# Optimization experiments

Measured on AMD Instinct MI355X. Metric: run time of the kernel, lower is better.

The kernel has to match this reference:

```python
import jax, jax.numpy as jnp
import numpy as np

B, N, T, C, H = 4, 1024, 32, 256, 8
LN_EPS = 1e-5


def setup_inputs() -> dict:
    key = jax.random.key(0)
    ks = jax.random.split(key, 10)
    BN = B * N
    x = jax.random.normal(ks[0], (BN, T, C), dtype=jnp.float32)
    # frame timestamps, sorted increasing, moderate scale so decay bias is meaningful
    timestamps = jnp.sort(jax.random.uniform(ks[1], (B, T), dtype=jnp.float32) * 64.0, axis=1)
    s = 0.02
    params = {
        'ln_gamma': jnp.ones((C,), jnp.float32),
        'ln_beta': jnp.zeros((C,), jnp.float32),
        'Wq': jax.random.normal(ks[2], (C, C), jnp.float32) * s,
        'bq': jnp.zeros((C,), jnp.float32),
        'Wk': jax.random.normal(ks[3], (C, C), jnp.float32) * s,
        'Wv': jax.random.normal(ks[4], (C, C), jnp.float32) * s,
        'Wg': jax.random.normal(ks[5], (C, C), jnp.float32) * s,
        # out_proj is zero-init in the module; use small random here so output is non-trivial
        'Wo': jax.random.normal(ks[6], (C, C), jnp.float32) * s,
        'log_lambda': jnp.linspace(np.log(0.004), np.log(0.7), H).astype(jnp.float32),
    }
    return {'x': x, 'timestamps': timestamps, 'n_spatial': N, **params}


def reference(x, timestamps, n_spatial, ln_gamma, ln_beta, Wq, bq, Wk, Wv, Wg, Wo, log_lambda):
    BN, T_, C_ = x.shape
    Bb = BN // n_spatial
    Hh = log_lambda.shape[0]
    d = C_ // Hh

    # LayerNorm
    mu = jnp.mean(x, axis=-1, keepdims=True)
    var = jnp.mean(jnp.square(x - mu), axis=-1, keepdims=True)
    h = (x - mu) * jax.lax.rsqrt(var + LN_EPS) * ln_gamma + ln_beta

    q = (h @ Wq.T + bq).reshape(BN, T_, Hh, d)
    k = (h @ Wk.T).reshape(BN, T_, Hh, d)
    v = (h @ Wv.T).reshape(BN, T_, Hh, d)
    g = jax.nn.sigmoid(h @ Wg.T)

    # temporal decay bias: (B, H, T, T), broadcast over spatial positions
    dt = jnp.abs(timestamps[:, :, None] - timestamps[:, None, :])  # (B,T,T)
    bias = -jnp.exp(log_lambda)[None, :, None, None] * dt[:, None, :, :]  # (B,H,T,T)

    scores = jnp.einsum('bthd,bshd->bhts', q.astype(jnp.float32), k.astype(jnp.float32))
    scores = scores / jnp.sqrt(jnp.float32(d))
    # broadcast bias instead of repeat_interleave: (B, N, H, T, T)
    scores = scores.reshape(Bb, n_spatial, Hh, T_, T_) + bias[:, None]
    attn = jax.nn.softmax(scores, axis=-1).reshape(BN, Hh, T_, T_)

    o = jnp.einsum('bhts,bshd->bthd', attn, v.astype(jnp.float32)).astype(v.dtype)
    o = o.reshape(BN, T_, C_)
    return x + (g * o) @ Wo.T
```

## Files before the change

kernel.cpp:

```cpp
#include <hip/hip_runtime.h>
#include <hip/hip_bf16.h>


typedef __attribute__((ext_vector_type(8))) short  s16x8;
typedef __attribute__((ext_vector_type(4))) float  f32x4;
typedef __attribute__((ext_vector_type(4))) unsigned short us16x4;

#define MFMA16(a, b, c) __builtin_amdgcn_mfma_f32_16x16x32_bf16((a), (b), (c), 0, 0, 0)

static __device__ __forceinline__ unsigned short f2bfu(float f) {
  __hip_bfloat16 h = __float2bfloat16(f);
  return __builtin_bit_cast(unsigned short, h);
}
static __device__ __forceinline__ unsigned pack2(float lo, float hi) {
  return (unsigned)f2bfu(lo) | ((unsigned)f2bfu(hi) << 16);
}
static __device__ __forceinline__ float bf_lo(unsigned u) {
  union { unsigned u; float f; } v; v.u = u << 16; return v.f;
}
static __device__ __forceinline__ float bf_hi(unsigned u) {
  union { unsigned u; float f; } v; v.u = u & 0xFFFF0000u; return v.f;
}

#define RS      528
#define ZSTR    72
#define LDS_A   0
#define LDS_TS  16896
#define LDS_Z   17024
#define ZONE    4608
#define LDS_TOTAL (LDS_Z + 4 * ZONE)

#define WS_WQ   0
#define WS_WK   131072
#define WS_WV   262144
#define WS_WG   393216
#define WS_WO   524288
#define WS_LAM  655360

__global__ void prep_kernel(const float* __restrict__ Wq, const float* __restrict__ Wk,
                            const float* __restrict__ Wv, const float* __restrict__ Wg,
                            const float* __restrict__ Wo, const float* __restrict__ ll,
                            char* __restrict__ ws) {
  int tid = blockIdx.x * 256 + threadIdx.x;
  if (tid < 5 * 8192) {
    int m      = tid >> 13;
    int within = tid & 8191;
    int lane   = within & 63;
    int j = 16 * (within >> 9) + (lane & 15);
    int c = 32 * ((within >> 6) & 7) + 8 * (lane >> 4);
    const float* W = (m == 0) ? Wq : (m == 1) ? Wk : (m == 2) ? Wv : (m == 3) ? Wg : Wo;
    const float* src = W + j * 256 + c;
    s16x8 o;
#pragma unroll
    for (int i = 0; i < 8; ++i) o[i] = (short)f2bfu(src[i]);
    *(s16x8*)(ws + (size_t)tid * 16) = o;
  } else if (tid < 5 * 8192 + 8) {
    ((float*)(ws + WS_LAM))[tid - 40960] = __expf(ll[tid - 40960]);
  }
}

template <int NT>
static __device__ __forceinline__ void gemmNT(const char* lds, const char* wmat,
                                              int ntg0, int lane, f32x4 acc[2][NT]) {
  const int l15 = lane & 15, l4 = lane >> 4;
  const s16x8* Bf = (const s16x8*)wmat + ntg0 * 8 * 64 + lane;
  s16x8 b[NT][8];
#pragma unroll
  for (int nt = 0; nt < NT; ++nt)
#pragma unroll
    for (int ks = 0; ks < 8; ++ks) b[nt][ks] = Bf[(nt * 8 + ks) * 64];
#pragma unroll
  for (int mt = 0; mt < 2; ++mt)
#pragma unroll
    for (int nt = 0; nt < NT; ++nt) acc[mt][nt] = (f32x4){0.f, 0.f, 0.f, 0.f};
#pragma unroll
  for (int ks = 0; ks < 8; ++ks) {
    s16x8 a[2];
#pragma unroll
    for (int mt = 0; mt < 2; ++mt)
      a[mt] = *(const s16x8*)(lds + LDS_A + (16 * mt + l15) * RS + 64 * ks + 16 * l4);
#pragma unroll
    for (int nt = 0; nt < NT; ++nt)
#pragma unroll
      for (int mt = 0; mt < 2; ++mt) acc[mt][nt] = MFMA16(a[mt], b[nt][ks], acc[mt][nt]);
  }
}

__global__ __launch_bounds__(256, 3) void fused_kernel(
    const float* __restrict__ x, const float* __restrict__ tsg,
    const float* __restrict__ gamma, const float* __restrict__ beta,
    const float* __restrict__ bq, const char* __restrict__ ws,
    float* __restrict__ out) {
  extern __shared__ __align__(16) char lds[];
  const int tid = threadIdx.x;
  const int lane = tid & 63;
  const int w = tid >> 6;
  const int l15 = lane & 15, l4 = lane >> 4;
  const int blk = blockIdx.x;
  char* zA = lds + LDS_Z + w * ZONE;
  char* zB = zA + 2304;

  {
    const int r = tid >> 3, sub = tid & 7;
    const float* xr = x + ((size_t)blk * 32 + r) * 256 + sub * 32;
    float4 xv[8];
    float s = 0.f, s2 = 0.f;
#pragma unroll
    for (int u = 0; u < 8; ++u) {
      xv[u] = *(const float4*)(xr + 4 * u);
      s  += xv[u].x + xv[u].y + xv[u].z + xv[u].w;
      s2 += xv[u].x * xv[u].x + xv[u].y * xv[u].y + xv[u].z * xv[u].z + xv[u].w * xv[u].w;
    }
#pragma unroll
    for (int m = 1; m <= 4; m <<= 1) { s += __shfl_xor(s, m); s2 += __shfl_xor(s2, m); }
    float mu = s * (1.f / 256.f);
    float rstd = rsqrtf(s2 * (1.f / 256.f) - mu * mu + 1e-5f);
#pragma unroll
    for (int u = 0; u < 8; ++u) {
      int c = sub * 32 + 4 * u;
      float4 gv = *(const float4*)(gamma + c);
      float4 bv = *(const float4*)(beta + c);
      us16x4 hb;
      hb[0] = f2bfu((xv[u].x - mu) * rstd * gv.x + bv.x);
      hb[1] = f2bfu((xv[u].y - mu) * rstd * gv.y + bv.y);
      hb[2] = f2bfu((xv[u].z - mu) * rstd * gv.z + bv.z);
      hb[3] = f2bfu((xv[u].w - mu) * rstd * gv.w + bv.w);
      *(us16x4*)(lds + LDS_A + r * RS + 2 * c) = hb;
    }
    if (tid < 32) ((float*)(lds + LDS_TS))[tid] = tsg[(blk >> 10) * 32 + tid];
  }
  __syncthreads();

  const float* tsl = (const float*)(lds + LDS_TS);
  const float* lam = (const float*)(ws + WS_LAM);
  const float tc0 = tsl[l15], tc1 = tsl[l15 + 16];
  float trow[8];
#pragma unroll
  for (int mh = 0; mh < 2; ++mh)
#pragma unroll
    for (int r = 0; r < 4; ++r) trow[mh * 4 + r] = tsl[16 * mh + 4 * l4 + r];
  const f32x4 zf = {0.f, 0.f, 0.f, 0.f};
  unsigned gopk[2][2][2][2];

#pragma unroll
  for (int hp = 0; hp < 2; ++hp) {
    const int h = 2 * w + hp;
    f32x4 acc[2][2];
    unsigned gpk[2][2][2];

    gemmNT<2>(lds, ws + WS_WG, 2 * h, lane, acc);
#pragma unroll
    for (int mt = 0; mt < 2; ++mt)
#pragma unroll
      for (int nt = 0; nt < 2; ++nt)
#pragma unroll
        for (int rp = 0; rp < 2; ++rp)
          gpk[mt][nt][rp] = pack2(1.f / (1.f + __expf(-acc[mt][nt][2 * rp])),
                                  1.f / (1.f + __expf(-acc[mt][nt][2 * rp + 1])));

    gemmNT<2>(lds, ws + WS_WV, 2 * h, lane, acc);
#pragma unroll
    for (int mt = 0; mt < 2; ++mt)
#pragma unroll
      for (int nt = 0; nt < 2; ++nt)
#pragma unroll
        for (int rp = 0; rp < 2; ++rp)
          *(unsigned*)(zB + (16 * nt + l15) * ZSTR + 2 * (16 * mt + 4 * l4 + 2 * rp)) =
              pack2(acc[mt][nt][2 * rp], acc[mt][nt][2 * rp + 1]);

    gemmNT<2>(lds, ws + WS_WK, 2 * h, lane, acc);
#pragma unroll
    for (int mt = 0; mt < 2; ++mt)
#pragma unroll
      for (int nt = 0; nt < 2; ++nt)
#pragma unroll
        for (int r = 0; r < 4; ++r)
          *(short*)(zA + (16 * mt + 4 * l4 + r) * ZSTR + 2 * (16 * nt + l15)) =
              (short)f2bfu(acc[mt][nt][r]);
    s16x8 bk0 = *(const s16x8*)(zA + l15 * ZSTR + 16 * l4);
    s16x8 bk1 = *(const s16x8*)(zA + (16 + l15) * ZSTR + 16 * l4);

    gemmNT<2>(lds, ws + WS_WQ, 2 * h, lane, acc);
    {
      float bq0 = bq[32 * h + l15], bq1 = bq[32 * h + 16 + l15];
#pragma unroll
      for (int mt = 0; mt < 2; ++mt)
#pragma unroll
        for (int nt = 0; nt < 2; ++nt)
#pragma unroll
          for (int r = 0; r < 4; ++r)
            *(short*)(zA + (16 * mt + 4 * l4 + r) * ZSTR + 2 * (16 * nt + l15)) =
                (short)f2bfu((acc[mt][nt][r] + (nt ? bq1 : bq0)) * 0.17677669529663687f);
    }
    s16x8 aq0 = *(const s16x8*)(zA + l15 * ZSTR + 16 * l4);
    s16x8 aq1 = *(const s16x8*)(zA + (16 + l15) * ZSTR + 16 * l4);

    f32x4 sc[2][2];
    sc[0][0] = MFMA16(aq0, bk0, zf);
    sc[0][1] = MFMA16(aq0, bk1, zf);
    sc[1][0] = MFMA16(aq1, bk0, zf);
    sc[1][1] = MFMA16(aq1, bk1, zf);

    const float lamh = lam[h];
#pragma unroll
    for (int mh = 0; mh < 2; ++mh)
#pragma unroll
      for (int r = 0; r < 4; ++r) {
        float tr = trow[mh * 4 + r];
        float a0 = sc[mh][0][r] - lamh * fabsf(tr - tc0);
        float a1 = sc[mh][1][r] - lamh * fabsf(tr - tc1);
        float m = fmaxf(a0, a1);
        m = fmaxf(m, __shfl_xor(m, 1)); m = fmaxf(m, __shfl_xor(m, 2));
        m = fmaxf(m, __shfl_xor(m, 4)); m = fmaxf(m, __shfl_xor(m, 8));
        float e0 = __expf(a0 - m), e1 = __expf(a1 - m);
        float su = e0 + e1;
        su += __shfl_xor(su, 1); su += __shfl_xor(su, 2);
        su += __shfl_xor(su, 4); su += __shfl_xor(su, 8);
        float inv = 1.0f / su;
        int t = 16 * mh + 4 * l4 + r;
        *(short*)(zA + t * ZSTR + 2 * l15)        = (short)f2bfu(e0 * inv);
        *(short*)(zA + t * ZSTR + 2 * (l15 + 16)) = (short)f2bfu(e1 * inv);
      }

    s16x8 ap0 = *(const s16x8*)(zA + l15 * ZSTR + 16 * l4);
    s16x8 ap1 = *(const s16x8*)(zA + (16 + l15) * ZSTR + 16 * l4);
    s16x8 bv0 = *(const s16x8*)(zB + l15 * ZSTR + 16 * l4);
    s16x8 bv1 = *(const s16x8*)(zB + (16 + l15) * ZSTR + 16 * l4);
#pragma unroll
    for (int mh = 0; mh < 2; ++mh)
#pragma unroll
      for (int nd = 0; nd < 2; ++nd) {
        f32x4 oa = MFMA16(mh ? ap1 : ap0, nd ? bv1 : bv0, zf);
#pragma unroll
        for (int rp = 0; rp < 2; ++rp) {
          unsigned gu = gpk[mh][nd][rp];
          gopk[hp][mh][nd][rp] =
              pack2(oa[2 * rp] * bf_lo(gu), oa[2 * rp + 1] * bf_hi(gu));
        }
      }
  }
  __syncthreads();

#pragma unroll
  for (int hp = 0; hp < 2; ++hp)
#pragma unroll
    for (int mh = 0; mh < 2; ++mh)
#pragma unroll
      for (int nd = 0; nd < 2; ++nd)
#pragma unroll
        for (int rp = 0; rp < 2; ++rp) {
          unsigned gu = gopk[hp][mh][nd][rp];
          int j = 32 * (2 * w + hp) + 16 * nd + l15;
          int r0 = 16 * mh + 4 * l4 + 2 * rp;
          *(short*)(lds + LDS_A + r0 * RS + 2 * j)       = (short)(gu & 0xFFFFu);
          *(short*)(lds + LDS_A + (r0 + 1) * RS + 2 * j) = (short)(gu >> 16);
        }
  __syncthreads();

#pragma unroll
  for (int half = 0; half < 2; ++half) {
    f32x4 facc[2][2];
    gemmNT<2>(lds, ws + WS_WO, 4 * w + 2 * half, lane, facc);
#pragma unroll
    for (int mt = 0; mt < 2; ++mt)
#pragma unroll
      for (int nt = 0; nt < 2; ++nt)
#pragma unroll
        for (int r = 0; r < 4; ++r) {
          int row = 16 * mt + 4 * l4 + r;
          int j = 64 * w + 32 * half + 16 * nt + l15;
          size_t gi = ((size_t)blk * 32 + row) * 256 + j;
          out[gi] = facc[mt][nt][r] + x[gi];
        }
  }
}

extern "C" void kernel_launch(void* const* d_in, const int* in_sizes, int n_in,
                              void* d_out, int out_size, void* d_ws, size_t ws_size,
                              hipStream_t stream) {
  const float* x     = (const float*)d_in[0];
  const float* ts    = (const float*)d_in[1];
  const float* gamma = (const float*)d_in[3];
  const float* beta  = (const float*)d_in[4];
  const float* Wq    = (const float*)d_in[5];
  const float* bq    = (const float*)d_in[6];
  const float* Wk    = (const float*)d_in[7];
  const float* Wv    = (const float*)d_in[8];
  const float* Wg    = (const float*)d_in[9];
  const float* Wo    = (const float*)d_in[10];
  const float* ll    = (const float*)d_in[11];
  char* ws   = (char*)d_ws;
  float* out = (float*)d_out;

  prep_kernel<<<161, 256, 0, stream>>>(Wq, Wk, Wv, Wg, Wo, ll, ws);

  (void)hipFuncSetAttribute((const void*)fused_kernel,
                            hipFuncAttributeMaxDynamicSharedMemorySize, LDS_TOTAL);
  fused_kernel<<<4096, 256, LDS_TOTAL, stream>>>(x, ts, gamma, beta, bq, ws, out);
}
```

Before: 429.3 us.

## Hoist LN activations into registers and interleave paired projection GEMMs

The bf16 LayerNorm activation fragments are loaded from LDS into registers once per wave and reused across all projection GEMMs, where before each gemmNT call reloaded them. The G/V and K/Q projections are computed in pairs with staggered weight loads, so global weight fetches overlap the MFMA chains. The much larger register footprint is accommodated by lowering the launch bound from 3 to 2 blocks per CU, which trades occupancy for fewer LDS reads and more memory-level parallelism.

```diff
diff --git a/kernel.cpp b/kernel.cpp
--- a/kernel.cpp
+++ b/kernel.cpp
@@ -86,7 +86,16 @@
   }
 }
 
-__global__ __launch_bounds__(256, 3) void fused_kernel(
+static __device__ __forceinline__ void quarter(const s16x8 ah[2][8], const s16x8 b[8],
+                                               f32x4 acc[2][2], int nt) {
+#pragma unroll
+  for (int ks = 0; ks < 8; ++ks)
+#pragma unroll
+    for (int mt = 0; mt < 2; ++mt)
+      acc[mt][nt] = MFMA16(ah[mt][ks], b[ks], acc[mt][nt]);
+}
+
+__global__ __launch_bounds__(256, 2) void fused_kernel(
     const float* __restrict__ x, const float* __restrict__ tsg,
     const float* __restrict__ gamma, const float* __restrict__ beta,
     const float* __restrict__ bq, const char* __restrict__ ws,
@@ -131,6 +140,13 @@
   }
   __syncthreads();
 
+  s16x8 ah[2][8];
+#pragma unroll
+  for (int mt = 0; mt < 2; ++mt)
+#pragma unroll
+    for (int ks = 0; ks < 8; ++ks)
+      ah[mt][ks] = *(const s16x8*)(lds + LDS_A + (16 * mt + l15) * RS + 64 * ks + 16 * l4);
+
   const float* tsl = (const float*)(lds + LDS_TS);
   const float* lam = (const float*)(ws + WS_LAM);
   const float tc0 = tsl[l15], tc1 = tsl[l15 + 16];
@@ -145,20 +161,40 @@
 #pragma unroll
   for (int hp = 0; hp < 2; ++hp) {
     const int h = 2 * w + hp;
-    f32x4 acc[2][2];
+    const s16x8* BG = (const s16x8*)(ws + WS_WG) + lane;
+    const s16x8* BV = (const s16x8*)(ws + WS_WV) + lane;
+    const s16x8* BK = (const s16x8*)(ws + WS_WK) + lane;
+    const s16x8* BQ = (const s16x8*)(ws + WS_WQ) + lane;
     unsigned gpk[2][2][2];
 
-    gemmNT<2>(lds, ws + WS_WG, 2 * h, lane, acc);
+    f32x4 accG[2][2], accV[2][2];
+    {
+      s16x8 bX0[8], bY0[8], bX1[8], bY1[8];
+#pragma unroll
+      for (int ks = 0; ks < 8; ++ks) bX0[ks] = BG[((2 * h + 0) * 8 + ks) * 64];
+#pragma unroll
+      for (int ks = 0; ks < 8; ++ks) bY0[ks] = BV[((2 * h + 0) * 8 + ks) * 64];
+#pragma unroll
+      for (int ks = 0; ks < 8; ++ks) bX1[ks] = BG[((2 * h + 1) * 8 + ks) * 64];
+#pragma unroll
+      for (int mt = 0; mt < 2; ++mt)
+#pragma unroll
+        for (int nt = 0; nt < 2; ++nt) { accG[mt][nt] = zf; accV[mt][nt] = zf; }
+      quarter(ah, bX0, accG, 0);
+#pragma unroll
+      for (int ks = 0; ks < 8; ++ks) bY1[ks] = BV[((2 * h + 1) * 8 + ks) * 64];
+      quarter(ah, bY0, accV, 0);
+      quarter(ah, bX1, accG, 1);
+      quarter(ah, bY1, accV, 1);
+    }
 #pragma unroll
     for (int mt = 0; mt < 2; ++mt)
 #pragma unroll
       for (int nt = 0; nt < 2; ++nt)
 #pragma unroll
         for (int rp = 0; rp < 2; ++rp)
-          gpk[mt][nt][rp] = pack2(1.f / (1.f + __expf(-acc[mt][nt][2 * rp])),
-                                  1.f / (1.f + __expf(-acc[mt][nt][2 * rp + 1])));
-
-    gemmNT<2>(lds, ws + WS_WV, 2 * h, lane, acc);
+          gpk[mt][nt][rp] = pack2(1.f / (1.f + __expf(-accG[mt][nt][2 * rp])),
+                                  1.f / (1.f + __expf(-accG[mt][nt][2 * rp + 1])));
 #pragma unroll
     for (int mt = 0; mt < 2; ++mt)
 #pragma unroll
@@ -166,9 +202,28 @@
 #pragma unroll
         for (int rp = 0; rp < 2; ++rp)
           *(unsigned*)(zB + (16 * nt + l15) * ZSTR + 2 * (16 * mt + 4 * l4 + 2 * rp)) =
-              pack2(acc[mt][nt][2 * rp], acc[mt][nt][2 * rp + 1]);
-
-    gemmNT<2>(lds, ws + WS_WK, 2 * h, lane, acc);
+              pack2(accV[mt][nt][2 * rp], accV[mt][nt][2 * rp + 1]);
+
+    f32x4 accK[2][2], accQ[2][2];
+    {
+      s16x8 bX0[8], bY0[8], bX1[8], bY1[8];
+#pragma unroll
+      for (int ks = 0; ks < 8; ++ks) bX0[ks] = BK[((2 * h + 0) * 8 + ks) * 64];
+#pragma unroll
+      for (int ks = 0; ks < 8; ++ks) bY0[ks] = BQ[((2 * h + 0) * 8 + ks) * 64];
+#pragma unroll
+      for (int ks = 0; ks < 8; ++ks) bX1[ks] = BK[((2 * h + 1) * 8 + ks) * 64];
+#pragma unroll
+      for (int mt = 0; mt < 2; ++mt)
+#pragma unroll
+        for (int nt = 0; nt < 2; ++nt) { accK[mt][nt] = zf; accQ[mt][nt] = zf; }
+      quarter(ah, bX0, accK, 0);
+#pragma unroll
+      for (int ks = 0; ks < 8; ++ks) bY1[ks] = BQ[((2 * h + 1) * 8 + ks) * 64];
+      quarter(ah, bY0, accQ, 0);
+      quarter(ah, bX1, accK, 1);
+      quarter(ah, bY1, accQ, 1);
+    }
 #pragma unroll
     for (int mt = 0; mt < 2; ++mt)
 #pragma unroll
@@ -176,11 +231,9 @@
 #pragma unroll
         for (int r = 0; r < 4; ++r)
           *(short*)(zA + (16 * mt + 4 * l4 + r) * ZSTR + 2 * (16 * nt + l15)) =
-              (short)f2bfu(acc[mt][nt][r]);
+              (short)f2bfu(accK[mt][nt][r]);
     s16x8 bk0 = *(const s16x8*)(zA + l15 * ZSTR + 16 * l4);
     s16x8 bk1 = *(const s16x8*)(zA + (16 + l15) * ZSTR + 16 * l4);
-
-    gemmNT<2>(lds, ws + WS_WQ, 2 * h, lane, acc);
     {
       float bq0 = bq[32 * h + l15], bq1 = bq[32 * h + 16 + l15];
 #pragma unroll
@@ -190,7 +243,7 @@
 #pragma unroll
           for (int r = 0; r < 4; ++r)
             *(short*)(zA + (16 * mt + 4 * l4 + r) * ZSTR + 2 * (16 * nt + l15)) =
-                (short)f2bfu((acc[mt][nt][r] + (nt ? bq1 : bq0)) * 0.17677669529663687f);
+                (short)f2bfu((accQ[mt][nt][r] + (nt ? bq1 : bq0)) * 0.17677669529663687f);
     }
     s16x8 aq0 = *(const s16x8*)(zA + l15 * ZSTR + 16 * l4);
     s16x8 aq1 = *(const s16x8*)(zA + (16 + l15) * ZSTR + 16 * l4);
```

New measurement: 521.7 us. 1.22x slower.
